# Optimization experiments

Hardware: AMD Instinct MI355X
Metric: run time of the kernel (lower is better)

Reference implementation:

```python
import jax, jax.numpy as jnp
import numpy as np

NZ = 128
N_GEN = 8
BATCH = 2048
SLOPE = 0.2


def _convt(x, w, b, stride, pad):
    # PyTorch ConvTranspose2d(weight [Cin,Cout,kH,kW], stride, padding p)
    # == conv with lhs_dilation=stride, padding=k-1-p, spatially-flipped
    # kernel with in/out channels swapped.
    k = jnp.flip(w, axis=(2, 3)).transpose(2, 3, 0, 1)  # [kH,kW,Cin,Cout]
    y = jax.lax.conv_general_dilated(
        x, k, window_strides=(1, 1), padding=[(pad, pad), (pad, pad)],
        lhs_dilation=(stride, stride),
        dimension_numbers=('NCHW', 'HWIO', 'NCHW'))
    return y + b[None, :, None, None]


def setup_inputs() -> dict:
    key = jax.random.key(0)
    ks = jax.random.split(key, 12)
    s = 0.05
    return {
        'z': jax.random.normal(ks[0], (BATCH, NZ), jnp.float32),
        'g_idx': jax.random.randint(ks[1], (BATCH,), 0, N_GEN),
        'W1': jax.random.normal(ks[2], (N_GEN, NZ, 256), jnp.float32) * s,
        'b1': jax.random.normal(ks[3], (N_GEN, 256), jnp.float32) * s,
        'W2': jax.random.normal(ks[4], (N_GEN, 256, 1568), jnp.float32) * s,
        'b2': jax.random.normal(ks[5], (N_GEN, 1568), jnp.float32) * s,
        'cw1': jax.random.normal(ks[6], (N_GEN, 32, 16, 4, 4), jnp.float32) * s,
        'cb1': jax.random.normal(ks[7], (N_GEN, 16), jnp.float32) * s,
        'cw2': jax.random.normal(ks[8], (N_GEN, 16, 8, 4, 4), jnp.float32) * s,
        'cb2': jax.random.normal(ks[9], (N_GEN, 8), jnp.float32) * s,
        'cw3': jax.random.normal(ks[10], (N_GEN, 8, 1, 3, 3), jnp.float32) * s,
        'cb3': jax.random.normal(ks[11], (N_GEN, 1), jnp.float32) * s,
    }


def _single_gen(params, z):
    W1, b1, W2, b2, cw1, cb1, cw2, cb2, cw3, cb3 = params
    lrelu = lambda x: jax.nn.leaky_relu(x, SLOPE)
    h = lrelu(z @ W1 + b1)                 # [B,256]
    h = lrelu(h @ W2 + b2)                 # [B,1568]
    h = h.reshape(-1, 32, 7, 7)
    h = lrelu(_convt(h, cw1, cb1, 2, 2))   # [B,16,14,14]
    h = lrelu(_convt(h, cw2, cb2, 2, 2))   # [B,8,28,28]
    return jnp.tanh(_convt(h, cw3, cb3, 1, 1))  # [B,1,28,28]


def reference(z, g_idx, W1, b1, W2, b2, cw1, cb1, cw2, cb2, cw3, cb3):
    params = (W1, b1, W2, b2, cw1, cb1, cw2, cb2, cw3, cb3)
    # Compute every generator on the full batch (faithful to the torch loop),
    # vmapped over the generator axis: images [G,B,1,28,28].
    images = jax.vmap(_single_gen, in_axes=((0,) * 10, None))(params, z)
    # Per-sample gather: keep generator g_idx[b] for each sample b.
    return images[g_idx, jnp.arange(z.shape[0])]
```

## Files before the change

kernel.cpp:

```cpp
#include <hip/hip_runtime.h>
#include <cstdint>
#include <cstddef>

#define BATCH 2048
#define NZ 128
#define NGEN 8
#define GRPS 32
#define MAXG 72
#define NCT 7
#define H2_ELEMS 1792
#define WS_H1_OFF 16384
#define WS_H2_OFF (16384 + MAXG * 8192 * 4)
#define WS_W2T_OFF (WS_H2_OFF + BATCH * H2_ELEMS * 2)
#define W2T_GSTRIDE (1568 * 256)
#define NB_W2T (NGEN * 49)
#define NB_PREP (NB_W2T + MAXG * 4)
#define WS_WPK1_OFF (WS_W2T_OFF + NGEN * W2T_GSTRIDE * 2)
#define WS_WPK2_OFF (WS_WPK1_OFF + NGEN * 4096 * 4)
#define WS_WPK3_OFF (WS_WPK2_OFF + NGEN * 1024 * 4)
#define PS 304

typedef unsigned int u32;
typedef unsigned short u16;
typedef unsigned long long u64;
typedef _Float16 f16x8 __attribute__((ext_vector_type(8)));
typedef _Float16 f16x4 __attribute__((ext_vector_type(4)));
typedef _Float16 f16x2 __attribute__((ext_vector_type(2)));
typedef float f32x4 __attribute__((ext_vector_type(4)));

__device__ __forceinline__ float lrelu(float x) { return fmaxf(x, 0.2f * x); }
__device__ __forceinline__ u16 f16b(float f) {
    _Float16 h = (_Float16)f;
    return __builtin_bit_cast(u16, h);
}
__device__ __forceinline__ u32 pk2(float a, float b) {
    f16x2 v; v[0] = (_Float16)a; v[1] = (_Float16)b;
    return __builtin_bit_cast(u32, v);
}
__device__ __forceinline__ float dot2(u32 a, u32 b, float c) {
#if __has_builtin(__builtin_amdgcn_fdot2)
    return __builtin_amdgcn_fdot2(__builtin_bit_cast(f16x2, a),
                                  __builtin_bit_cast(f16x2, b), c, false);
#else
    float d;
    asm("v_dot2_f32_f16 %0, %1, %2, %3" : "=v"(d) : "v"(a), "v"(b), "v"(c));
    return d;
#endif
}
__device__ __forceinline__ float fast_tanh(float x) {
    x = fminf(fmaxf(x, -9.f), 9.f);
    const float e = __expf(2.f * x);
    return (e - 1.f) / (e + 1.f);
}
__device__ __forceinline__ int h2off(int n) {
    const int ci = n / 49, rm = n % 49;
    return ci * 56 + (rm / 7) * 8 + (rm % 7);
}

__global__ __launch_bounds__(256) void prep_kernel(
    const float* __restrict__ z, const int* __restrict__ g_idx,
    const float* __restrict__ W1, const float* __restrict__ b1,
    const float* __restrict__ W2, int* __restrict__ wsi,
    float* __restrict__ h1g, _Float16* __restrict__ W2T,
    const float* __restrict__ cw1, const float* __restrict__ cw2,
    const float* __restrict__ cw3,
    u32* __restrict__ wpk1, u32* __restrict__ wpk2, u32* __restrict__ wpk3)
{
    __shared__ __align__(16) char pmem[16896];

    const int tid = threadIdx.x;
    const int bx = blockIdx.x;

    if (bx < NB_W2T) {
        _Float16 (*t)[264] = (_Float16 (*)[264])pmem;
        const int g = bx / 49;
        const int n0 = (bx % 49) * 32;
        const float* src = W2 + (size_t)g * 256 * 1568;
        const int nl = tid & 31, kh = tid >> 5;
        #pragma unroll 8
        for (int p = 0; p < 32; ++p) {
            const int k = p * 8 + kh;
            t[nl][k] = (_Float16)src[(size_t)k * 1568 + n0 + nl];
        }
        __syncthreads();
        _Float16* dst = W2T + (size_t)g * W2T_GSTRIDE + (size_t)n0 * 256;
        #pragma unroll
        for (int ii = 0; ii < 4; ++ii) {
            const int i = tid + 256 * ii;
            const int n = i >> 5, kc = i & 31;
            *(uint4*)(dst + (size_t)n * 256 + kc * 8) = *(const uint4*)&t[n][kc * 8];
        }
        return;
    }

    if (bx >= NB_PREP && bx < NB_PREP + NGEN) {
        const int g = bx - NB_PREP;
        const float* c1p = cw1 + g * 8192;
        u32* o1 = wpk1 + g * 4096;
        for (int i = tid; i < 4096; i += 256) {
            const int cip = i >> 8, a = (i >> 6) & 3, co = (i >> 2) & 15, c = i & 3;
            const float* s = c1p + cip * 512 + co * 16 + a * 4 + c;
            o1[i] = pk2(s[0], s[256]);
        }
        const float* c2p = cw2 + g * 2048;
        u32* o2 = wpk2 + g * 1024;
        for (int i = tid; i < 1024; i += 256) {
            const int cip = i >> 7, a = (i >> 5) & 3, co = (i >> 2) & 7, c = i & 3;
            const float* s = c2p + cip * 256 + co * 16 + a * 4 + c;
            o2[i] = pk2(s[0], s[128]);
        }
        if (tid < 36) {
            const int cip = tid / 9, r = tid % 9;
            const float* s = cw3 + g * 72 + cip * 18 + r;
            wpk3[g * 36 + tid] = pk2(s[0], s[9]);
        }
        return;
    }

    u16* rank       = (u16*)pmem;
    int (*wcnt)[NGEN]  = (int (*)[NGEN])(pmem + 4096);
    int (*wboff)[NGEN] = (int (*)[NGEN])(pmem + 4224);
    int* pbase      = (int*)(pmem + 4352);
    const int w = tid >> 6, lane = tid & 63;
    if (tid < 4 * NGEN) wcnt[tid >> 3][tid & 7] = 0;
    __syncthreads();
    const u64 lt = ((u64)1 << lane) - 1;
    #pragma unroll
    for (int r = 0; r < 8; ++r) {
        const int b = r * 256 + tid;
        const int gg = g_idx[b];
        u64 m[NGEN];
        #pragma unroll
        for (int k = 0; k < NGEN; ++k) m[k] = __ballot(gg == k);
        rank[b] = (u16)((int)__popcll(m[gg] & lt) + wcnt[w][gg]);
        if (lane < NGEN) wcnt[w][lane] += (int)__popcll(m[lane]);
    }
    __syncthreads();
    if (tid == 0) {
        int acc = 0;
        for (int g = 0; g < NGEN; ++g) {
            pbase[g] = acc;
            const int tot = wcnt[0][g] + wcnt[1][g] + wcnt[2][g] + wcnt[3][g];
            acc += ((tot + GRPS - 1) / GRPS) * GRPS;
        }
        pbase[NGEN] = acc;
    }
    __syncthreads();
    if (tid < 32) {
        const int ww = tid >> 3, g = tid & 7;
        int off = pbase[g];
        for (int w2 = 0; w2 < ww; ++w2) off += wcnt[w2][g];
        wboff[ww][g] = off;
    }
    __syncthreads();

    if (bx >= NB_PREP + NGEN) {
        if (tid == 0) wsi[0] = pbase[NGEN];
        for (int i = tid; i < MAXG * GRPS; i += 256) wsi[16 + i] = -1;
        __syncthreads();
        #pragma unroll
        for (int r = 0; r < 8; ++r) {
            const int b = r * 256 + tid;
            const int gg = g_idx[b];
            wsi[16 + wboff[w][gg] + (int)rank[b]] = b;
        }
        return;
    }

    const int bx2 = bx - NB_W2T;
    const int grp = bx2 >> 2;
    const int s0 = (bx2 & 3) * 8;
    if (grp * GRPS >= pbase[NGEN]) return;

    int gsel = 0;
    #pragma unroll
    for (int g = 1; g < NGEN; ++g) if (grp * GRPS >= pbase[g]) gsel = g;

    int* sb = (int*)(pmem + 4400);
    float (*zst)[12] = (float (*)[12])(pmem + 4608);
    if (tid < 8) sb[tid] = -1;
    __syncthreads();
    const int base = grp * GRPS + s0;
    #pragma unroll
    for (int r = 0; r < 8; ++r) {
        const int b = r * 256 + tid;
        const int gg = g_idx[b];
        const int rel = wboff[w][gg] + (int)rank[b] - base;
        if ((unsigned)rel < 8u) sb[rel] = b;
    }
    __syncthreads();

    const float* W1g = W1 + gsel * (NZ * 256);
    const float* b1g = b1 + gsel * 256;

    {
        const int s = tid >> 5, f = tid & 31;
        float4 v = make_float4(0.f, 0.f, 0.f, 0.f);
        if (sb[s] >= 0) v = *(const float4*)(z + (size_t)sb[s] * NZ + 4 * f);
        zst[4 * f + 0][s] = v.x; zst[4 * f + 1][s] = v.y;
        zst[4 * f + 2][s] = v.z; zst[4 * f + 3][s] = v.w;
    }
    __syncthreads();

    const int c = tid;
    float acc[8];
    #pragma unroll
    for (int s = 0; s < 8; ++s) acc[s] = 0.f;
    const float* wp = W1g + c;
    #pragma unroll 4
    for (int k = 0; k < NZ; ++k) {
        const float wv = wp[k * 256];
        float av[8];
        *(float4*)&av[0] = *(const float4*)&zst[k][0];
        *(float4*)&av[4] = *(const float4*)&zst[k][4];
        #pragma unroll
        for (int s = 0; s < 8; ++s) acc[s] += av[s] * wv;
    }
    const float bv = b1g[c];
    float* hp = h1g + (size_t)grp * 8192 + (size_t)s0 * 256 + c;
    #pragma unroll
    for (int s = 0; s < 8; ++s) hp[s * 256] = lrelu(acc[s] + bv);
}

__global__ __launch_bounds__(256) void fc2_kernel(
    const int* __restrict__ g_idx,
    const _Float16* __restrict__ W2T, const float* __restrict__ b2,
    const int* __restrict__ wsi, const float* __restrict__ h1g,
    u16* __restrict__ h2g)
{
    __shared__ __align__(16) char afsm[GRPS * PS * 2];
    _Float16* afrag = (_Float16*)afsm;
    __shared__ int sb[GRPS];
    __shared__ int sG;

    const int tid = threadIdx.x;
    const int grp = blockIdx.x / NCT;
    const int tile = blockIdx.x % NCT;
    if (grp * GRPS >= wsi[0]) return;

    if (tid == 0) sG = g_idx[wsi[16 + grp * GRPS]];
    if (tid < GRPS) sb[tid] = wsi[16 + grp * GRPS + tid];
    __syncthreads();
    const _Float16* W2Tg = W2T + (size_t)sG * W2T_GSTRIDE;
    const float* b2g = b2 + sG * 1568;

    {
        const float4* h1p4 = (const float4*)(h1g + (size_t)grp * 8192);
        #pragma unroll
        for (int i = 0; i < 8; ++i) {
            const int u = tid + 256 * i;
            const int j4 = u & 1;
            const int ln = (u >> 1) & 63;
            const int kq = (u >> 7) & 7;
            const int mt = (u >> 10) & 1;
            const int s = mt * 16 + (ln & 15);
            const float4 v = h1p4[s * 64 + kq * 8 + ((ln >> 4) << 1) + j4];
            f16x4 hi;
            hi[0] = (_Float16)v.x; hi[1] = (_Float16)v.y;
            hi[2] = (_Float16)v.z; hi[3] = (_Float16)v.w;
            const int bh = ((mt * 8 + kq) * 64 + ln) * 8 + 4 * j4;
            *(f16x4*)&afrag[bh] = hi;
        }
    }
    __syncthreads();

    const int wave = tid >> 6;
    const int lane = tid & 63;
    const int q = lane >> 4;
    const int nl = lane & 15;
    const int nbw = tile * 256 + wave * 64;

    f32x4 accA[4], accB[4];
    #pragma unroll
    for (int nt = 0; nt < 4; ++nt) {
        accA[nt] = (f32x4){0.f, 0.f, 0.f, 0.f};
        accB[nt] = accA[nt];
    }
    #pragma unroll
    for (int nt = 0; nt < 4; ++nt) {
        const int nb = nbw + nt * 16;
        if (nb < 1568) {
            const _Float16* bp = W2Tg + (size_t)(nb + nl) * 256 + q * 8;
            #pragma unroll
            for (int kq = 0; kq < 8; ++kq) {
                const f16x8 b = *(const f16x8*)(bp + kq * 32);
                const f16x8 a0 = *(const f16x8*)&afrag[((0 * 8 + kq) * 64 + lane) * 8];
                const f16x8 a1 = *(const f16x8*)&afrag[((1 * 8 + kq) * 64 + lane) * 8];
                accA[nt] = __builtin_amdgcn_mfma_f32_16x16x32_f16(a0, b, accA[nt], 0, 0, 0);
                accB[nt] = __builtin_amdgcn_mfma_f32_16x16x32_f16(a1, b, accB[nt], 0, 0, 0);
            }
        }
    }
    __syncthreads();

    u16* pst = (u16*)afsm;
    const int nstart = tile * 256;
    const int nend = (nstart + 256 < 1568) ? nstart + 256 : 1568;
    const int offLo = h2off(nstart), offHi = h2off(nend - 1);
    const int lo8 = offLo & ~7;

    #pragma unroll
    for (int nt = 0; nt < 4; ++nt) {
        const int nb = nbw + nt * 16;
        if (nb < 1568) {
            const int n = nb + nl;
            const float bias = b2g[n];
            u16* pp = pst + (h2off(n) - lo8);
            #pragma unroll
            for (int reg = 0; reg < 4; ++reg) {
                pp[(q * 4 + reg) * PS]      = f16b(lrelu(accA[nt][reg] + bias));
                pp[(16 + q * 4 + reg) * PS] = f16b(lrelu(accB[nt][reg] + bias));
            }
        }
    }
    __syncthreads();

    {
        const int s = tid >> 3, p = tid & 7;
        const int bb = sb[s];
        if (bb >= 0) {
            u16* row = h2g + (size_t)bb * H2_ELEMS;
            const u16* ps = pst + s * PS - lo8;
            const int c0 = (offLo + 7) & ~7;
            const int c1 = (offHi + 1) & ~7;
            for (int o = offLo + p; o < c0 && o <= offHi; o += 8) row[o] = ps[o];
            const int t0 = (c1 > offLo) ? c1 : offLo;
            for (int o = t0 + p; o <= offHi; o += 8) row[o] = ps[o];
            for (int c = c0 + p * 8; c + 8 <= c1; c += 64)
                *(uint4*)(row + c) = *(const uint4*)(ps + c);
        }
    }
}

__device__ __forceinline__ void conv2p_full(
    const u32 (*c1s)[14][20], u16* dst,
    const u32* __restrict__ w2g, const float bv, const int co, const int y)
{
    float acc[28];
    #pragma unroll
    for (int x = 0; x < 28; ++x) acc[x] = bv;
    const int a0 = (y + 1) & 1;
    for (int aa = 0; aa < 2; ++aa) {
        const int a = a0 + 2 * aa;
        const int iy = (y + 1 - a) >> 1;
        if ((unsigned)iy < 14u) {
            #pragma unroll 2
            for (int cip = 0; cip < 8; ++cip) {
                u32 rr[14];
                *(uint4*)&rr[0]  = *(const uint4*)&c1s[cip][iy][0];
                *(uint4*)&rr[4]  = *(const uint4*)&c1s[cip][iy][4];
                *(uint4*)&rr[8]  = *(const uint4*)&c1s[cip][iy][8];
                *(uint2*)&rr[12] = *(const uint2*)&c1s[cip][iy][12];
                const uint4 wq = *(const uint4*)(w2g + ((cip * 4 + a) * 8 + co) * 4);
                const u32 wv[4] = {wq.x, wq.y, wq.z, wq.w};
                #pragma unroll
                for (int x = 0; x < 28; ++x) {
                    const int c0v = (x + 1) & 1;
                    const int ix0 = (x + 1 - c0v) >> 1;
                    if (ix0 < 14) acc[x] = dot2(rr[ix0],     wv[c0v],     acc[x]);
                    if (ix0 >= 1) acc[x] = dot2(rr[ix0 - 1], wv[c0v + 2], acc[x]);
                }
            }
        }
    }
    #pragma unroll
    for (int x = 0; x < 28; ++x) dst[2 * (1 + x)] = f16b(lrelu(acc[x]));
}

__global__ __launch_bounds__(256, 6) void conv_kernel(
    const int* __restrict__ g_idx, const int* __restrict__ wsi,
    const u32* __restrict__ wpk1, const float* __restrict__ cb1,
    const u32* __restrict__ wpk2, const float* __restrict__ cb2,
    const u32* __restrict__ wpk3, const float* __restrict__ cb3,
    const u16* __restrict__ h2g, float* __restrict__ out)
{
    __shared__ __align__(16) char smem[8960 + 13440];
    u32 (*c1s)[14][20] = (u32 (*)[14][20])smem;
    u32 (*h2s)[7][8]   = (u32 (*)[7][8])(smem + 8960);
    u32 (*c2s)[28][30] = (u32 (*)[28][30])(smem + 8960);
    __shared__ u32 w3s[36];

    const int tid = threadIdx.x;
    const int b = wsi[16 + blockIdx.x];
    if (b < 0) return;
    const int g = g_idx[b];
    const u32* w1g = wpk1 + g * 4096;
    const u32* w2g = wpk2 + g * 1024;
    const float* cb1g = cb1 + g * 16;
    const float* cb2g = cb2 + g * 8;
    const float  cb3v = cb3[g];

    if (tid < 224) {
        const uint4 qv = ((const uint4*)(h2g + (size_t)b * H2_ELEMS))[tid];
        const int ci = tid / 7, yq = tid % 7;
        u16* dst = (u16*)&h2s[ci >> 1][yq][0] + (ci & 1);
        const u32 w[4] = {qv.x, qv.y, qv.z, qv.w};
        #pragma unroll
        for (int j = 0; j < 4; ++j) {
            dst[4 * j]     = (u16)(w[j] & 0xffffu);
            dst[4 * j + 2] = (u16)(w[j] >> 16);
        }
    }
    if (tid < 36) w3s[tid] = wpk3[g * 36 + tid];
    __syncthreads();

    if (tid < 224) {
        const int co = tid / 14, y = tid % 14;
        const float bv = cb1g[co];
        float acc[14];
        #pragma unroll
        for (int x = 0; x < 14; ++x) acc[x] = bv;
        const int a0 = (y + 1) & 1;
        for (int aa = 0; aa < 2; ++aa) {
            const int a = a0 + 2 * aa;
            const int iy = (y + 1 - a) >> 1;
            if ((unsigned)iy < 7u) {
                #pragma unroll 2
                for (int cip = 0; cip < 16; ++cip) {
                    u32 rr[8];
                    *(uint4*)&rr[0] = *(const uint4*)&h2s[cip][iy][0];
                    *(uint4*)&rr[4] = *(const uint4*)&h2s[cip][iy][4];
                    const uint4 wq = *(const uint4*)(w1g + ((cip * 4 + a) * 16 + co) * 4);
                    const u32 wv[4] = {wq.x, wq.y, wq.z, wq.w};
                    #pragma unroll
                    for (int x = 0; x < 14; ++x) {
                        const int c0v = (x + 1) & 1;
                        const int ix0 = (x + 1 - c0v) >> 1;
                        if (ix0 < 7)  acc[x] = dot2(rr[ix0],     wv[c0v],     acc[x]);
                        if (ix0 >= 1) acc[x] = dot2(rr[ix0 - 1], wv[c0v + 2], acc[x]);
                    }
                }
            }
        }
        u16* dst = (u16*)&c1s[co >> 1][y][0] + (co & 1);
        #pragma unroll
        for (int x = 0; x < 14; ++x) dst[2 * x] = f16b(lrelu(acc[x]));
    }
    __syncthreads();

    if (tid < 224) {
        const int zc = tid / 56, zr = tid % 56;
        c2s[zc][zr % 28][(zr < 28) ? 0 : 29] = 0u;
        const int co = tid / 28, y = tid % 28;
        const float bv = cb2g[co];
        u16* dst = (u16*)&c2s[co >> 1][y][0] + (co & 1);
        conv2p_full(c1s, dst, w2g, bv, co, y);
    }
    __syncthreads();

    if (tid < 196) {
        const int y = tid / 7, qq = tid % 7;
        const int xb = qq * 4;
        float acc[4] = {cb3v, cb3v, cb3v, cb3v};
        #pragma unroll 2
        for (int cip = 0; cip < 4; ++cip) {
            u32 wp[9];
            #pragma unroll
            for (int j = 0; j < 9; ++j) wp[j] = w3s[cip * 9 + j];
            #pragma unroll
            for (int a = 0; a < 3; ++a) {
                const int iy = y + 1 - a;
                if ((unsigned)iy < 28u) {
                    u32 rr[6];
                    *(uint2*)&rr[0] = *(const uint2*)&c2s[cip][iy][xb];
                    *(uint2*)&rr[2] = *(const uint2*)&c2s[cip][iy][xb + 2];
                    *(uint2*)&rr[4] = *(const uint2*)&c2s[cip][iy][xb + 4];
                    #pragma unroll
                    for (int xx = 0; xx < 4; ++xx)
                        #pragma unroll
                        for (int c = 0; c < 3; ++c)
                            acc[xx] = dot2(rr[xx + 2 - c], wp[a * 3 + c], acc[xx]);
                }
            }
        }
        float* op = out + (size_t)b * 784 + y * 28 + xb;
        #pragma unroll
        for (int xx = 0; xx < 4; ++xx) op[xx] = fast_tanh(acc[xx]);
    }
}

extern "C" void kernel_launch(void* const* d_in, const int* in_sizes, int n_in,
                              void* d_out, int out_size, void* d_ws, size_t ws_size,
                              hipStream_t stream) {
    const float* z   = (const float*)d_in[0];
    const int*   gi  = (const int*)d_in[1];
    const float* W1  = (const float*)d_in[2];
    const float* b1  = (const float*)d_in[3];
    const float* W2  = (const float*)d_in[4];
    const float* b2  = (const float*)d_in[5];
    const float* cw1 = (const float*)d_in[6];
    const float* cb1 = (const float*)d_in[7];
    const float* cw2 = (const float*)d_in[8];
    const float* cb2 = (const float*)d_in[9];
    const float* cw3 = (const float*)d_in[10];
    const float* cb3 = (const float*)d_in[11];
    int*      wsi = (int*)d_ws;
    float*    h1g = (float*)((char*)d_ws + WS_H1_OFF);
    u16*      h2g = (u16*)((char*)d_ws + WS_H2_OFF);
    _Float16* w2t = (_Float16*)((char*)d_ws + WS_W2T_OFF);
    u32*      wpk1 = (u32*)((char*)d_ws + WS_WPK1_OFF);
    u32*      wpk2 = (u32*)((char*)d_ws + WS_WPK2_OFF);
    u32*      wpk3 = (u32*)((char*)d_ws + WS_WPK3_OFF);

    prep_kernel<<<NB_PREP + NGEN + 1, 256, 0, stream>>>(z, gi, W1, b1, W2, wsi,
                                                        h1g, w2t, cw1, cw2, cw3,
                                                        wpk1, wpk2, wpk3);
    fc2_kernel<<<MAXG * NCT, 256, 0, stream>>>(gi, w2t, b2, wsi, h1g, h2g);
    conv_kernel<<<MAXG * GRPS, 256, 0, stream>>>(gi, wsi, wpk1, cb1, wpk2, cb2,
                                                 wpk3, cb3, h2g, (float*)d_out);
}
```

Baseline: 160.6 us.

## Compute first transposed conv with MFMA via stride-2 phase decomposition

Replaces the scalar dot2 loop for the first ConvTranspose layer with MFMA 16x16x32 f16 instructions. Each wave handles one output parity phase (py,px), and the four contributing taps become K=32 channel matmuls over 49 output positions. The prep kernel repacks cw1 into a per-phase, per-tap f16 A-operand layout, and the h2 tile in shared memory gets a zero-padded 9x10 halo so no boundary checks are needed. In exchange it adds strided scalar LDS gathers for the B operand, extra zero-fill work, and 2-byte scattered stores into c1s.

```diff
diff --git a/kernel.cpp b/kernel.cpp
--- a/kernel.cpp
+++ b/kernel.cpp
@@ -16,7 +16,7 @@
 #define NB_W2T (NGEN * 49)
 #define NB_PREP (NB_W2T + MAXG * 4)
 #define WS_WPK1_OFF (WS_W2T_OFF + NGEN * W2T_GSTRIDE * 2)
-#define WS_WPK2_OFF (WS_WPK1_OFF + NGEN * 4096 * 4)
+#define WS_WPK2_OFF (WS_WPK1_OFF + NGEN * 8192 * 2)
 #define WS_WPK3_OFF (WS_WPK2_OFF + NGEN * 1024 * 4)
 #define PS 304
 
@@ -64,7 +64,7 @@
     float* __restrict__ h1g, _Float16* __restrict__ W2T,
     const float* __restrict__ cw1, const float* __restrict__ cw2,
     const float* __restrict__ cw3,
-    u32* __restrict__ wpk1, u32* __restrict__ wpk2, u32* __restrict__ wpk3)
+    u16* __restrict__ apk1, u32* __restrict__ wpk2, u32* __restrict__ wpk3)
 {
     __shared__ __align__(16) char pmem[16896];
 
@@ -96,11 +96,13 @@
     if (bx >= NB_PREP && bx < NB_PREP + NGEN) {
         const int g = bx - NB_PREP;
         const float* c1p = cw1 + g * 8192;
-        u32* o1 = wpk1 + g * 4096;
-        for (int i = tid; i < 4096; i += 256) {
-            const int cip = i >> 8, a = (i >> 6) & 3, co = (i >> 2) & 15, c = i & 3;
-            const float* s = c1p + cip * 512 + co * 16 + a * 4 + c;
-            o1[i] = pk2(s[0], s[256]);
+        u16* o1 = apk1 + g * 8192;
+        for (int i = tid; i < 8192; i += 256) {
+            const int ci = i & 31, co = (i >> 5) & 15, t = (i >> 9) & 3;
+            const int px = (i >> 11) & 1, py = (i >> 12) & 1;
+            const int a = 1 - py + 2 * (t >> 1);
+            const int c = 1 - px + 2 * (t & 1);
+            o1[i] = f16b(c1p[ci * 256 + co * 16 + a * 4 + c]);
         }
         const float* c2p = cw2 + g * 2048;
         u32* o2 = wpk2 + g * 1024;
@@ -369,72 +371,102 @@
 
 __global__ __launch_bounds__(256, 6) void conv_kernel(
     const int* __restrict__ g_idx, const int* __restrict__ wsi,
-    const u32* __restrict__ wpk1, const float* __restrict__ cb1,
+    const u16* __restrict__ apk1, const float* __restrict__ cb1,
     const u32* __restrict__ wpk2, const float* __restrict__ cb2,
     const u32* __restrict__ wpk3, const float* __restrict__ cb3,
     const u16* __restrict__ h2g, float* __restrict__ out)
 {
     __shared__ __align__(16) char smem[8960 + 13440];
     u32 (*c1s)[14][20] = (u32 (*)[14][20])smem;
-    u32 (*h2s)[7][8]   = (u32 (*)[7][8])(smem + 8960);
+    u32 (*h2s)[9][10]  = (u32 (*)[9][10])(smem + 8960);
     u32 (*c2s)[28][30] = (u32 (*)[28][30])(smem + 8960);
     __shared__ u32 w3s[36];
+    __shared__ float sc1[16];
 
     const int tid = threadIdx.x;
     const int b = wsi[16 + blockIdx.x];
     if (b < 0) return;
     const int g = g_idx[b];
-    const u32* w1g = wpk1 + g * 4096;
+    const u16* a1g = apk1 + g * 8192;
     const u32* w2g = wpk2 + g * 1024;
-    const float* cb1g = cb1 + g * 16;
     const float* cb2g = cb2 + g * 8;
     const float  cb3v = cb3[g];
 
+    for (int i = tid; i < 656; i += 256) {
+        const int cip = i / 41, rem = i % 41;
+        int r, c;
+        if (rem < 10)      { r = 0; c = rem; }
+        else if (rem < 20) { r = 8; c = rem - 10; }
+        else { const int j = rem - 20; r = 1 + j / 3;
+               const int jm = j % 3; c = (jm == 0) ? 0 : (jm == 1 ? 8 : 9); }
+        h2s[cip][r][c] = 0u;
+    }
     if (tid < 224) {
         const uint4 qv = ((const uint4*)(h2g + (size_t)b * H2_ELEMS))[tid];
         const int ci = tid / 7, yq = tid % 7;
-        u16* dst = (u16*)&h2s[ci >> 1][yq][0] + (ci & 1);
+        u16* dst = (u16*)&h2s[ci >> 1][yq + 1][1] + (ci & 1);
         const u32 w[4] = {qv.x, qv.y, qv.z, qv.w};
         #pragma unroll
-        for (int j = 0; j < 4; ++j) {
+        for (int j = 0; j < 3; ++j) {
             dst[4 * j]     = (u16)(w[j] & 0xffffu);
             dst[4 * j + 2] = (u16)(w[j] >> 16);
         }
+        dst[12] = (u16)(w[3] & 0xffffu);
     }
     if (tid < 36) w3s[tid] = wpk3[g * 36 + tid];
-    __syncthreads();
-
-    if (tid < 224) {
-        const int co = tid / 14, y = tid % 14;
-        const float bv = cb1g[co];
-        float acc[14];
-        #pragma unroll
-        for (int x = 0; x < 14; ++x) acc[x] = bv;
-        const int a0 = (y + 1) & 1;
-        for (int aa = 0; aa < 2; ++aa) {
-            const int a = a0 + 2 * aa;
-            const int iy = (y + 1 - a) >> 1;
-            if ((unsigned)iy < 7u) {
-                #pragma unroll 2
-                for (int cip = 0; cip < 16; ++cip) {
-                    u32 rr[8];
-                    *(uint4*)&rr[0] = *(const uint4*)&h2s[cip][iy][0];
-                    *(uint4*)&rr[4] = *(const uint4*)&h2s[cip][iy][4];
-                    const uint4 wq = *(const uint4*)(w1g + ((cip * 4 + a) * 16 + co) * 4);
-                    const u32 wv[4] = {wq.x, wq.y, wq.z, wq.w};
-                    #pragma unroll
-                    for (int x = 0; x < 14; ++x) {
-                        const int c0v = (x + 1) & 1;
-                        const int ix0 = (x + 1 - c0v) >> 1;
-                        if (ix0 < 7)  acc[x] = dot2(rr[ix0],     wv[c0v],     acc[x]);
-                        if (ix0 >= 1) acc[x] = dot2(rr[ix0 - 1], wv[c0v + 2], acc[x]);
-                    }
+    if (tid < 16) sc1[tid] = cb1[g * 16 + tid];
+    __syncthreads();
+
+    {
+        const int wv_ = tid >> 6;
+        const int py = wv_ >> 1, px = wv_ & 1;
+        const int lane = tid & 63;
+        const int n = lane & 15;
+        const int q = lane >> 4;
+        const u16* ag = a1g + ((py * 2 + px) * 4) * 512 + n * 32 + q * 8;
+        f16x8 af[4];
+        #pragma unroll
+        for (int t = 0; t < 4; ++t) af[t] = *(const f16x8*)(ag + t * 512);
+
+        int oyv[4], oxv[4];
+        #pragma unroll
+        for (int tile = 0; tile < 4; ++tile) {
+            int p = tile * 16 + n; if (p > 48) p = 48;
+            oyv[tile] = p / 7; oxv[tile] = p % 7;
+        }
+        f32x4 acc[4];
+        #pragma unroll
+        for (int tile = 0; tile < 4; ++tile) acc[tile] = (f32x4){0.f, 0.f, 0.f, 0.f};
+
+        #pragma unroll
+        for (int t = 0; t < 4; ++t) {
+            const int dy = py - (t >> 1) + 1;
+            const int dx = px - (t & 1) + 1;
+            #pragma unroll
+            for (int tile = 0; tile < 4; ++tile) {
+                const int r = oyv[tile] + dy, c = oxv[tile] + dx;
+                uint4 bw;
+                bw.x = h2s[q * 4 + 0][r][c];
+                bw.y = h2s[q * 4 + 1][r][c];
+                bw.z = h2s[q * 4 + 2][r][c];
+                bw.w = h2s[q * 4 + 3][r][c];
+                acc[tile] = __builtin_amdgcn_mfma_f32_16x16x32_f16(
+                    af[t], __builtin_bit_cast(f16x8, bw), acc[tile], 0, 0, 0);
+            }
+        }
+        #pragma unroll
+        for (int tile = 0; tile < 4; ++tile) {
+            const int pos = tile * 16 + n;
+            if (pos < 49) {
+                const int y = 2 * oyv[tile] + py, x = 2 * oxv[tile] + px;
+                #pragma unroll
+                for (int reg = 0; reg < 4; ++reg) {
+                    const int m = q * 4 + reg;
+                    u16* d = (u16*)&c1s[m >> 1][y][x] + (m & 1);
+                    *d = f16b(lrelu(acc[tile][reg] + sc1[m]));
                 }
             }
         }
-        u16* dst = (u16*)&c1s[co >> 1][y][0] + (co & 1);
-        #pragma unroll
-        for (int x = 0; x < 14; ++x) dst[2 * x] = f16b(lrelu(acc[x]));
     }
     __syncthreads();
 
@@ -498,14 +530,14 @@
     float*    h1g = (float*)((char*)d_ws + WS_H1_OFF);
     u16*      h2g = (u16*)((char*)d_ws + WS_H2_OFF);
     _Float16* w2t = (_Float16*)((char*)d_ws + WS_W2T_OFF);
-    u32*      wpk1 = (u32*)((char*)d_ws + WS_WPK1_OFF);
+    u16*      apk1 = (u16*)((char*)d_ws + WS_WPK1_OFF);
     u32*      wpk2 = (u32*)((char*)d_ws + WS_WPK2_OFF);
     u32*      wpk3 = (u32*)((char*)d_ws + WS_WPK3_OFF);
 
     prep_kernel<<<NB_PREP + NGEN + 1, 256, 0, stream>>>(z, gi, W1, b1, W2, wsi,
                                                         h1g, w2t, cw1, cw2, cw3,
-                                                        wpk1, wpk2, wpk3);
+                                                        apk1, wpk2, wpk3);
     fc2_kernel<<<MAXG * NCT, 256, 0, stream>>>(gi, w2t, b2, wsi, h1g, h2g);
-    conv_kernel<<<MAXG * GRPS, 256, 0, stream>>>(gi, wsi, wpk1, cb1, wpk2, cb2,
+    conv_kernel<<<MAXG * GRPS, 256, 0, stream>>>(gi, wsi, apk1, cb1, wpk2, cb2,
                                                  wpk3, cb3, h2g, (float*)d_out);
 }
```

Result: faster. 148.4 us (-7.6%).
